# Kernel optimization log

Hardware: AMD Instinct MI355X
Metric: run time of the kernel (lower is better)

The kernel has to match this reference:

```python
import jax, jax.numpy as jnp
import numpy as np

SPATIAL_SHAPES = ((128, 128), (64, 64), (32, 32), (16, 16))  # (h, w) per level
N_HEADS, N_LEVELS, N_POINTS, D_MODEL = 8, 4, 4, 256


def setup_inputs() -> dict:
    key = jax.random.key(0)
    ks = jax.random.split(key, 10)
    bs, nq, nk = 4, 300, 17
    inp = {
        'query': jax.random.normal(ks[0], (bs, nq * nk, D_MODEL), jnp.float32),
        'reference_points': jax.random.uniform(ks[1], (bs, nq, N_LEVELS, nk, 2), jnp.float32),
    }
    for l, (h, w) in enumerate(SPATIAL_SHAPES):
        inp[f'value{l}'] = jax.random.normal(ks[2 + l], (bs * N_HEADS, D_MODEL // N_HEADS, h * w), jnp.float32)
    inp['W_off'] = jax.random.normal(ks[6], (N_HEADS * N_LEVELS * N_POINTS * 2, D_MODEL), jnp.float32) * 0.02
    inp['b_off'] = jax.random.normal(ks[7], (N_HEADS * N_LEVELS * N_POINTS * 2,), jnp.float32) * 0.5
    inp['W_attn'] = jax.random.normal(ks[8], (N_HEADS * N_LEVELS * N_POINTS, D_MODEL), jnp.float32) * 0.02
    inp['b_attn'] = jax.random.normal(ks[9], (N_HEADS * N_LEVELS * N_POINTS,), jnp.float32) * 0.02
    return inp


def _bilinear_sample(v, grid, h, w):
    # v: (N, C, h*w); grid: (N, P, 2) normalized to [-1, 1] (x, y).
    # F.grid_sample bilinear, padding_mode='zeros', align_corners=False.
    x = (grid[..., 0] + 1.0) * 0.5 * w - 0.5
    y = (grid[..., 1] + 1.0) * 0.5 * h - 0.5
    x0 = jnp.floor(x)
    y0 = jnp.floor(y)
    wx1, wy1 = x - x0, y - y0
    wx0, wy0 = 1.0 - wx1, 1.0 - wy1
    x0i, y0i = x0.astype(jnp.int32), y0.astype(jnp.int32)
    out = 0.0
    for xi, yi, wgt in ((x0i, y0i, wx0 * wy0), (x0i + 1, y0i, wx1 * wy0),
                        (x0i, y0i + 1, wx0 * wy1), (x0i + 1, y0i + 1, wx1 * wy1)):
        valid = (xi >= 0) & (xi < w) & (yi >= 0) & (yi < h)
        idx = jnp.clip(yi, 0, h - 1) * w + jnp.clip(xi, 0, w - 1)       # (N, P)
        g = jnp.take_along_axis(v, idx[:, None, :], axis=2)              # (N, C, P)
        out = out + g * (wgt * valid.astype(v.dtype))[:, None, :]
    return out


def reference(query, reference_points, value0, value1, value2, value3, W_off, b_off, W_attn, b_attn):
    bs, len_q, _ = query.shape
    hd = D_MODEL // N_HEADS
    values = (value0, value1, value2, value3)

    off = (query @ W_off.T + b_off).reshape(bs, len_q, N_HEADS, N_LEVELS, N_POINTS, 2)
    attn = (query @ W_attn.T + b_attn).reshape(bs, len_q, N_HEADS, N_LEVELS * N_POINTS)
    attn = jax.nn.softmax(attn, axis=-1)

    # (bs, nq, L, nk, 2) -> transpose(2,3) -> flatten(1,2) -> (bs, len_q, L, 2)
    rp = jnp.transpose(reference_points, (0, 1, 3, 2, 4)).reshape(bs, len_q, N_LEVELS, 2)
    # normalizer: spatial (h, w) flipped -> (w, h)
    norm = jnp.array([[w, h] for (h, w) in SPATIAL_SHAPES], dtype=query.dtype).reshape(1, 1, 1, N_LEVELS, 1, 2)
    loc = rp[:, :, None, :, None, :] + off / norm                         # (bs, len_q, H, L, P, 2)

    grids = 2.0 * loc - 1.0
    grids = jnp.transpose(grids, (0, 2, 1, 3, 4, 5)).reshape(bs * N_HEADS, len_q, N_LEVELS, N_POINTS, 2)

    sampled = []
    for l, (h, w) in enumerate(SPATIAL_SHAPES):
        g = grids[:, :, l].reshape(bs * N_HEADS, len_q * N_POINTS, 2)
        s = _bilinear_sample(values[l], g, h, w)                          # (bs*H, hd, len_q*P)
        sampled.append(s.reshape(bs * N_HEADS, hd, len_q, N_POINTS))
    sampled = jnp.concatenate(sampled, axis=-1)                           # (bs*H, hd, len_q, L*P)

    attn_r = jnp.transpose(attn, (0, 2, 1, 3)).reshape(bs * N_HEADS, 1, len_q, N_LEVELS * N_POINTS)
    out = (sampled * attn_r).sum(-1).reshape(bs, D_MODEL, len_q)
    return jnp.transpose(out, (0, 2, 1))                                  # (bs, len_q, d_model)
```

## Files before the change

kernel.cpp:

```cpp
#include <hip/hip_runtime.h>
#include <math.h>

#define BS        4
#define NQ        300
#define NK        17
#define LEN_Q     5100
#define N_HEADS   8
#define N_LEVELS  4
#define N_POINTS  4
#define D_MODEL   256
#define HD        32

#define LB0 0
#define LB1 16777216
#define LB2 20971520
#define LB3 22020096
#define VT_TOTAL 22282240
#define PROJ_F32 7833600
#define QB_N     5222400

#define NTRANS 21760
#define NCVT   2598

typedef __attribute__((ext_vector_type(8))) short bf16x8;
typedef __attribute__((ext_vector_type(8))) unsigned short ushort8_t;
typedef __attribute__((ext_vector_type(4))) float f32x4;
typedef __attribute__((ext_vector_type(4))) unsigned int u32x4;

__device__ __forceinline__ unsigned short f2bf(float x) {
    unsigned u = __float_as_uint(x);
    unsigned r = (u + 0x7fffu + ((u >> 16) & 1u)) >> 16;
    return (unsigned short)r;
}
__device__ __forceinline__ float bf2f(unsigned short s) {
    return __uint_as_float((unsigned)s << 16);
}
__device__ __forceinline__ float dot2bf(unsigned v, unsigned w, float acc) {
    float r;
    asm("v_dot2_f32_bf16 %0, %1, %2, %3" : "=v"(r) : "v"(v), "v"(w), "v"(acc));
    return r;
}

__global__ __launch_bounds__(256) void prep_kernel(
    const float* __restrict__ v0, const float* __restrict__ v1,
    const float* __restrict__ v2, const float* __restrict__ v3,
    const float* __restrict__ Q, const float* __restrict__ Woff,
    const float* __restrict__ Wattn,
    unsigned short* __restrict__ vt,
    unsigned short* __restrict__ Qb, unsigned short* __restrict__ Wb)
{
    __shared__ float t[32][36];
    int bid = blockIdx.x;
    int tid = threadIdx.x;

    if (bid < NTRANS) {
        int bx = bid % 680;
        int n  = bid / 680;
        const float* in; int S; size_t ob; int tile;
        if (bx < 512)      { in = v0; S = 16384; ob = LB0; tile = bx; }
        else if (bx < 640) { in = v1; S = 4096;  ob = LB1; tile = bx - 512; }
        else if (bx < 672) { in = v2; S = 1024;  ob = LB2; tile = bx - 640; }
        else               { in = v3; S = 256;   ob = LB3; tile = bx - 672; }

        int s0 = tile * 32;
        int c  = tid >> 3;
        int c4 = (tid & 7) * 4;
        const float* pin = in + (size_t)n * 32 * S;
        *(float4*)&t[c][c4] = *(const float4*)(pin + (size_t)c * S + s0 + c4);
        __syncthreads();

        unsigned short* pout = vt + ob + (size_t)n * S * 32;
        int r = tid >> 3;
        ushort4 w;
        w.x = f2bf(t[c4 + 0][r]);
        w.y = f2bf(t[c4 + 1][r]);
        w.z = f2bf(t[c4 + 2][r]);
        w.w = f2bf(t[c4 + 3][r]);
        *(ushort4*)(pout + (size_t)(s0 + r) * 32 + c4) = w;
    } else {
        int gid = (bid - NTRANS) * 256 + tid;
        const float* src;
        unsigned short* dst;
        size_t off;
        if (gid < 652800) {
            src = Q; dst = Qb; off = (size_t)gid * 8;
        } else {
            int wg = gid - 652800;
            off = (size_t)wg * 8;
            dst = Wb;
            if (off < 65536) { src = Woff; }
            else             { src = Wattn; src -= 65536; }
        }
        float4 a = *(const float4*)(src + off);
        float4 b = *(const float4*)(src + off + 4);
        ushort8_t r;
        r[0] = f2bf(a.x); r[1] = f2bf(a.y); r[2] = f2bf(a.z); r[3] = f2bf(a.w);
        r[4] = f2bf(b.x); r[5] = f2bf(b.y); r[6] = f2bf(b.z); r[7] = f2bf(b.w);
        *(ushort8_t*)(dst + off) = r;
    }
}

__global__ __launch_bounds__(256) void proj_gemm_mfma(
    const unsigned short* __restrict__ Qb,
    const unsigned short* __restrict__ Wb,
    const float* __restrict__ boff, const float* __restrict__ battn,
    float* __restrict__ P, int M)
{
    int tid  = threadIdx.x;
    int wave = tid >> 6;
    int lane = tid & 63;
    int bm = blockIdx.y * 64;
    int bn = blockIdx.x * 64;
    int wm = (wave & 1) * 32;
    int wn = (wave >> 1) * 32;
    int lr = lane & 15;
    int lk = (lane >> 4) * 8;

    int ra0 = bm + wm + lr;       ra0 = ra0 < M ? ra0 : M - 1;
    int ra1 = bm + wm + 16 + lr;  ra1 = ra1 < M ? ra1 : M - 1;
    const unsigned short* qa0 = Qb + (size_t)ra0 * 256 + lk;
    const unsigned short* qa1 = Qb + (size_t)ra1 * 256 + lk;
    const unsigned short* wb0 = Wb + (size_t)(bn + wn + lr) * 256 + lk;
    const unsigned short* wb1 = Wb + (size_t)(bn + wn + 16 + lr) * 256 + lk;

    f32x4 acc[2][2] = {};
    #pragma unroll
    for (int k0 = 0; k0 < 256; k0 += 32) {
        bf16x8 a0 = *(const bf16x8*)(qa0 + k0);
        bf16x8 a1 = *(const bf16x8*)(qa1 + k0);
        bf16x8 b0 = *(const bf16x8*)(wb0 + k0);
        bf16x8 b1 = *(const bf16x8*)(wb1 + k0);
        acc[0][0] = __builtin_amdgcn_mfma_f32_16x16x32_bf16(a0, b0, acc[0][0], 0, 0, 0);
        acc[0][1] = __builtin_amdgcn_mfma_f32_16x16x32_bf16(a0, b1, acc[0][1], 0, 0, 0);
        acc[1][0] = __builtin_amdgcn_mfma_f32_16x16x32_bf16(a1, b0, acc[1][0], 0, 0, 0);
        acc[1][1] = __builtin_amdgcn_mfma_f32_16x16x32_bf16(a1, b1, acc[1][1], 0, 0, 0);
    }

    #pragma unroll
    for (int i = 0; i < 2; ++i) {
        int mbase = bm + wm + i * 16 + (lane >> 4) * 4;
        #pragma unroll
        for (int j = 0; j < 2; ++j) {
            int n = bn + wn + j * 16 + (lane & 15);
            float bias = (n < 256) ? boff[n] : battn[n - 256];
            #pragma unroll
            for (int r = 0; r < 4; ++r) {
                int row = mbase + r;
                if (row < M) P[(size_t)row * 384 + n] = acc[i][j][r] + bias;
            }
        }
    }
}

#define GLD(dst, base, off)                                                  \
    { const unsigned short* _p = (base) + (off);                             \
      asm volatile("global_load_dwordx4 %0, %1, off"                         \
                   : "=v"(dst) : "v"(_p)); }

#define DOT2P(C0, C1, wpk)                                                   \
  a0 = dot2bf(__builtin_amdgcn_perm(C1[0], C0[0], 0x05040100u), wpk, a0);    \
  a1 = dot2bf(__builtin_amdgcn_perm(C1[0], C0[0], 0x07060302u), wpk, a1);    \
  a2 = dot2bf(__builtin_amdgcn_perm(C1[1], C0[1], 0x05040100u), wpk, a2);    \
  a3 = dot2bf(__builtin_amdgcn_perm(C1[1], C0[1], 0x07060302u), wpk, a3);    \
  a4 = dot2bf(__builtin_amdgcn_perm(C1[2], C0[2], 0x05040100u), wpk, a4);    \
  a5 = dot2bf(__builtin_amdgcn_perm(C1[2], C0[2], 0x07060302u), wpk, a5);    \
  a6 = dot2bf(__builtin_amdgcn_perm(C1[3], C0[3], 0x05040100u), wpk, a6);    \
  a7 = dot2bf(__builtin_amdgcn_perm(C1[3], C0[3], 0x07060302u), wpk, a7);

#define RED(v) { v += __shfl_xor(v, 4); v += __shfl_xor(v, 8); }

__global__ __launch_bounds__(256, 4) void ms_deform_kernel(
    const float* __restrict__ rp,
    const float* __restrict__ proj,
    const unsigned short* __restrict__ vt,
    float* __restrict__ out)
{
    int bid = blockIdx.x;
    int h   = bid & 7;
    int b   = (bid >> 3) & 3;
    int qc  = bid >> 5;
    int q0  = qc * 16;

    __shared__ int s_iw[3104];

    int tid = threadIdx.x;

    {
        int qL = tid >> 4;
        int lp = tid & 15;
        int l  = lp >> 2;
        int p  = lp & 3;
        int q  = q0 + qL;
        int qq = q < LEN_Q ? q : LEN_Q - 1;
        const float* prow = proj + (size_t)(b * LEN_Q + qq) * 384;

        float g = prow[256 + h * 16 + lp];
        float mx = g;
        mx = fmaxf(mx, __shfl_xor(mx, 1, 16));
        mx = fmaxf(mx, __shfl_xor(mx, 2, 16));
        mx = fmaxf(mx, __shfl_xor(mx, 4, 16));
        mx = fmaxf(mx, __shfl_xor(mx, 8, 16));
        float e = __expf(g - mx);
        float s = e;
        s += __shfl_xor(s, 1, 16);
        s += __shfl_xor(s, 2, 16);
        s += __shfl_xor(s, 4, 16);
        s += __shfl_xor(s, 8, 16);
        float a = (q < LEN_Q) ? (e / s) : 0.f;

        int Wl = 128 >> l;
        float ww = (float)Wl;
        int qi = qq / NK;
        int ki = qq - qi * NK;
        size_t rbase = ((((size_t)b * NQ + qi) * N_LEVELS + l) * NK + ki) * 2;
        float rx = rp[rbase + 0];
        float ry = rp[rbase + 1];
        int oj = (h * 16 + lp) * 2;
        float ox = prow[oj], oy = prow[oj + 1];
        float x = (rx + ox / ww) * ww - 0.5f;
        float y = (ry + oy / ww) * ww - 0.5f;
        float x0f = floorf(x), y0f = floorf(y);
        float wx1 = x - x0f, wy1 = y - y0f;
        float wx0 = 1.f - wx1, wy0 = 1.f - wy1;
        int x0 = (int)x0f, y0 = (int)y0f;

        int idx[4]; float wf[4];
        #pragma unroll
        for (int corner = 0; corner < 4; ++corner) {
            int xi = x0 + (corner & 1);
            int yi = y0 + (corner >> 1);
            float wgt = ((corner & 1) ? wx1 : wx0) * ((corner >> 1) ? wy1 : wy0);
            bool valid = (xi >= 0) && (xi < Wl) && (yi >= 0) && (yi < Wl);
            idx[corner] = valid ? (yi * Wl + xi) * HD : 0;
            wf[corner]  = valid ? wgt * a : 0.f;
        }
        int* wrow = s_iw + (qL >> 1) * 388 + (p * 8 + l * 2 + (qL & 1)) * 12;
        *(int4*)wrow = make_int4(idx[0], idx[1], idx[2], idx[3]);
        unsigned wpkA = ((unsigned)f2bf(wf[1]) << 16) | f2bf(wf[0]);
        unsigned wpkB = ((unsigned)f2bf(wf[3]) << 16) | f2bf(wf[2]);
        *(int2*)(wrow + 4) = make_int2((int)wpkA, (int)wpkB);
    }
    __builtin_amdgcn_wave_barrier();

    int qL = tid >> 4;
    int l  = (tid >> 2) & 3;
    int c8 = tid & 3;
    int n  = b * N_HEADS + h;
    const size_t lb[4]  = {LB0, LB1, LB2, LB3};
    const int    Ssz[4] = {16384, 4096, 1024, 256};

    const unsigned short* vbase = vt + lb[l] + (size_t)n * Ssz[l] * HD + c8 * 8;
    const int* rrow0 = s_iw + (qL >> 1) * 388 + (l * 2 + (qL & 1)) * 12;

    int4 I0 = *(const int4*)(rrow0 + 0);
    int2 W0 = *(const int2*)(rrow0 + 4);
    int4 I1 = *(const int4*)(rrow0 + 96);
    int2 W1 = *(const int2*)(rrow0 + 100);
    int4 I2 = *(const int4*)(rrow0 + 192);
    int2 W2 = *(const int2*)(rrow0 + 196);
    int4 I3 = *(const int4*)(rrow0 + 288);
    int2 W3 = *(const int2*)(rrow0 + 292);

    u32x4 u00, u01, u02, u03, u10, u11, u12, u13;
    u32x4 u20, u21, u22, u23, u30, u31, u32, u33;
    GLD(u00, vbase, I0.x) GLD(u01, vbase, I0.y)
    GLD(u02, vbase, I0.z) GLD(u03, vbase, I0.w)
    GLD(u10, vbase, I1.x) GLD(u11, vbase, I1.y)
    GLD(u12, vbase, I1.z) GLD(u13, vbase, I1.w)
    GLD(u20, vbase, I2.x) GLD(u21, vbase, I2.y)
    GLD(u22, vbase, I2.z) GLD(u23, vbase, I2.w)
    GLD(u30, vbase, I3.x) GLD(u31, vbase, I3.y)
    GLD(u32, vbase, I3.z) GLD(u33, vbase, I3.w)
    asm volatile("s_waitcnt vmcnt(0)"
        : "+v"(u00), "+v"(u01), "+v"(u02), "+v"(u03),
          "+v"(u10), "+v"(u11), "+v"(u12), "+v"(u13),
          "+v"(u20), "+v"(u21), "+v"(u22), "+v"(u23),
          "+v"(u30), "+v"(u31), "+v"(u32), "+v"(u33));
    __builtin_amdgcn_sched_barrier(0);

    float a0 = 0.f, a1 = 0.f, a2 = 0.f, a3 = 0.f;
    float a4 = 0.f, a5 = 0.f, a6 = 0.f, a7 = 0.f;
    DOT2P(u00, u01, ((unsigned)W0.x))
    DOT2P(u02, u03, ((unsigned)W0.y))
    DOT2P(u10, u11, ((unsigned)W1.x))
    DOT2P(u12, u13, ((unsigned)W1.y))
    DOT2P(u20, u21, ((unsigned)W2.x))
    DOT2P(u22, u23, ((unsigned)W2.y))
    DOT2P(u30, u31, ((unsigned)W3.x))
    DOT2P(u32, u33, ((unsigned)W3.y))

    RED(a0) RED(a1) RED(a2) RED(a3) RED(a4) RED(a5) RED(a6) RED(a7)

    if ((tid & 12) == 0) {
        int q = q0 + qL;
        if (q < LEN_Q) {
            float* po = out + (size_t)(b * LEN_Q + q) * 256 + h * 32 + c8 * 8;
            float4 oA = make_float4(a0, a1, a2, a3);
            float4 oB = make_float4(a4, a5, a6, a7);
            *(float4*)po = oA;
            *(float4*)(po + 4) = oB;
        }
    }
}

extern "C" void kernel_launch(void* const* d_in, const int* in_sizes, int n_in,
                              void* d_out, int out_size, void* d_ws, size_t ws_size,
                              hipStream_t stream)
{
    const float* query = (const float*)d_in[0];
    const float* refp  = (const float*)d_in[1];
    const float* v0    = (const float*)d_in[2];
    const float* v1    = (const float*)d_in[3];
    const float* v2    = (const float*)d_in[4];
    const float* v3    = (const float*)d_in[5];
    const float* Woff  = (const float*)d_in[6];
    const float* boff  = (const float*)d_in[7];
    const float* Wattn = (const float*)d_in[8];
    const float* battn = (const float*)d_in[9];
    float* out = (float*)d_out;
    unsigned short* vt = (unsigned short*)d_ws;
    float* proj = (float*)(vt + VT_TOTAL);
    unsigned short* Qb = (unsigned short*)(proj + PROJ_F32);
    unsigned short* Wb = Qb + QB_N;

    int M = BS * LEN_Q;

    prep_kernel<<<NTRANS + NCVT, 256, 0, stream>>>(
        v0, v1, v2, v3, query, Woff, Wattn, vt, Qb, Wb);

    proj_gemm_mfma<<<dim3(6, (M + 63) / 64), 256, 0, stream>>>(
        Qb, Wb, boff, battn, proj, M);

    ms_deform_kernel<<<319 * 32, 256, 0, stream>>>(refp, proj, vt, out);
}
```

Before: 105.9 us.

## Fuse projection GEMM into deformable sampling kernel via per-block MFMA

Removes the separate projection GEMM kernel and its fp32 intermediate buffer. Each sampling block now computes, with bf16 MFMA on three waves, the 48 projection columns its head needs for its 16 queries and stages them in shared memory. This saves a kernel launch and the write and re-read of the projection matrix. The cost is an extra barrier, one idle wave during the GEMM phase, and more shared memory per block, which may lower occupancy.

```diff
diff --git a/kernel.cpp b/kernel.cpp
--- a/kernel.cpp
+++ b/kernel.cpp
@@ -16,7 +16,6 @@
 #define LB2 20971520
 #define LB3 22020096
 #define VT_TOTAL 22282240
-#define PROJ_F32 7833600
 #define QB_N     5222400
 
 #define NTRANS 21760
@@ -100,58 +99,6 @@
     }
 }
 
-__global__ __launch_bounds__(256) void proj_gemm_mfma(
-    const unsigned short* __restrict__ Qb,
-    const unsigned short* __restrict__ Wb,
-    const float* __restrict__ boff, const float* __restrict__ battn,
-    float* __restrict__ P, int M)
-{
-    int tid  = threadIdx.x;
-    int wave = tid >> 6;
-    int lane = tid & 63;
-    int bm = blockIdx.y * 64;
-    int bn = blockIdx.x * 64;
-    int wm = (wave & 1) * 32;
-    int wn = (wave >> 1) * 32;
-    int lr = lane & 15;
-    int lk = (lane >> 4) * 8;
-
-    int ra0 = bm + wm + lr;       ra0 = ra0 < M ? ra0 : M - 1;
-    int ra1 = bm + wm + 16 + lr;  ra1 = ra1 < M ? ra1 : M - 1;
-    const unsigned short* qa0 = Qb + (size_t)ra0 * 256 + lk;
-    const unsigned short* qa1 = Qb + (size_t)ra1 * 256 + lk;
-    const unsigned short* wb0 = Wb + (size_t)(bn + wn + lr) * 256 + lk;
-    const unsigned short* wb1 = Wb + (size_t)(bn + wn + 16 + lr) * 256 + lk;
-
-    f32x4 acc[2][2] = {};
-    #pragma unroll
-    for (int k0 = 0; k0 < 256; k0 += 32) {
-        bf16x8 a0 = *(const bf16x8*)(qa0 + k0);
-        bf16x8 a1 = *(const bf16x8*)(qa1 + k0);
-        bf16x8 b0 = *(const bf16x8*)(wb0 + k0);
-        bf16x8 b1 = *(const bf16x8*)(wb1 + k0);
-        acc[0][0] = __builtin_amdgcn_mfma_f32_16x16x32_bf16(a0, b0, acc[0][0], 0, 0, 0);
-        acc[0][1] = __builtin_amdgcn_mfma_f32_16x16x32_bf16(a0, b1, acc[0][1], 0, 0, 0);
-        acc[1][0] = __builtin_amdgcn_mfma_f32_16x16x32_bf16(a1, b0, acc[1][0], 0, 0, 0);
-        acc[1][1] = __builtin_amdgcn_mfma_f32_16x16x32_bf16(a1, b1, acc[1][1], 0, 0, 0);
-    }
-
-    #pragma unroll
-    for (int i = 0; i < 2; ++i) {
-        int mbase = bm + wm + i * 16 + (lane >> 4) * 4;
-        #pragma unroll
-        for (int j = 0; j < 2; ++j) {
-            int n = bn + wn + j * 16 + (lane & 15);
-            float bias = (n < 256) ? boff[n] : battn[n - 256];
-            #pragma unroll
-            for (int r = 0; r < 4; ++r) {
-                int row = mbase + r;
-                if (row < M) P[(size_t)row * 384 + n] = acc[i][j][r] + bias;
-            }
-        }
-    }
-}
-
 #define GLD(dst, base, off)                                                  \
     { const unsigned short* _p = (base) + (off);                             \
       asm volatile("global_load_dwordx4 %0, %1, off"                         \
@@ -171,7 +118,9 @@
 
 __global__ __launch_bounds__(256, 4) void ms_deform_kernel(
     const float* __restrict__ rp,
-    const float* __restrict__ proj,
+    const unsigned short* __restrict__ Qb,
+    const unsigned short* __restrict__ Wb,
+    const float* __restrict__ boff, const float* __restrict__ battn,
     const unsigned short* __restrict__ vt,
     float* __restrict__ out)
 {
@@ -181,9 +130,41 @@
     int qc  = bid >> 5;
     int q0  = qc * 16;
 
-    __shared__ int s_iw[3104];
+    __shared__ int   s_iw[3104];
+    __shared__ float s_proj[16][52];
 
     int tid = threadIdx.x;
+
+    {
+        int wave = tid >> 6;
+        int lane = tid & 63;
+        if (wave < 3) {
+            int tbase = (wave == 0) ? h * 32
+                      : (wave == 1) ? h * 32 + 16
+                                    : 256 + h * 16;
+            int lr = lane & 15;
+            int lk = (lane >> 4) * 8;
+            int qrow = q0 + lr; qrow = qrow < LEN_Q ? qrow : LEN_Q - 1;
+            const unsigned short* qa = Qb + ((size_t)b * LEN_Q + qrow) * 256 + lk;
+            const unsigned short* wb = Wb + (size_t)(tbase + lr) * 256 + lk;
+            f32x4 acc = {};
+            #pragma unroll
+            for (int k0 = 0; k0 < 256; k0 += 32) {
+                bf16x8 af = *(const bf16x8*)(qa + k0);
+                bf16x8 bf = *(const bf16x8*)(wb + k0);
+                acc = __builtin_amdgcn_mfma_f32_16x16x32_bf16(af, bf, acc, 0, 0, 0);
+            }
+            int col = lane & 15;
+            int ncol = tbase + col;
+            float bias = (ncol < 256) ? boff[ncol] : battn[ncol - 256];
+            int lcol = wave * 16 + col;
+            int rb2 = (lane >> 4) * 4;
+            #pragma unroll
+            for (int r = 0; r < 4; ++r)
+                s_proj[rb2 + r][lcol] = acc[r] + bias;
+        }
+    }
+    __syncthreads();
 
     {
         int qL = tid >> 4;
@@ -192,9 +173,8 @@
         int p  = lp & 3;
         int q  = q0 + qL;
         int qq = q < LEN_Q ? q : LEN_Q - 1;
-        const float* prow = proj + (size_t)(b * LEN_Q + qq) * 384;
-
-        float g = prow[256 + h * 16 + lp];
+
+        float g = s_proj[qL][32 + lp];
         float mx = g;
         mx = fmaxf(mx, __shfl_xor(mx, 1, 16));
         mx = fmaxf(mx, __shfl_xor(mx, 2, 16));
@@ -215,8 +195,8 @@
         size_t rbase = ((((size_t)b * NQ + qi) * N_LEVELS + l) * NK + ki) * 2;
         float rx = rp[rbase + 0];
         float ry = rp[rbase + 1];
-        int oj = (h * 16 + lp) * 2;
-        float ox = prow[oj], oy = prow[oj + 1];
+        float ox = s_proj[qL][lp * 2];
+        float oy = s_proj[qL][lp * 2 + 1];
         float x = (rx + ox / ww) * ww - 0.5f;
         float y = (ry + oy / ww) * ww - 0.5f;
         float x0f = floorf(x), y0f = floorf(y);
@@ -319,17 +299,12 @@
     const float* battn = (const float*)d_in[9];
     float* out = (float*)d_out;
     unsigned short* vt = (unsigned short*)d_ws;
-    float* proj = (float*)(vt + VT_TOTAL);
-    unsigned short* Qb = (unsigned short*)(proj + PROJ_F32);
+    unsigned short* Qb = vt + VT_TOTAL;
     unsigned short* Wb = Qb + QB_N;
-
-    int M = BS * LEN_Q;
 
     prep_kernel<<<NTRANS + NCVT, 256, 0, stream>>>(
         v0, v1, v2, v3, query, Woff, Wattn, vt, Qb, Wb);
 
-    proj_gemm_mfma<<<dim3(6, (M + 63) / 64), 256, 0, stream>>>(
-        Qb, Wb, boff, battn, proj, M);
-
-    ms_deform_kernel<<<319 * 32, 256, 0, stream>>>(refp, proj, vt, out);
-}
+    ms_deform_kernel<<<319 * 32, 256, 0, stream>>>(
+        refp, Qb, Wb, boff, battn, vt, out);
+}
```

After: 114.5 us. 1.08x slower.
